# Optimization experiments

Hardware: AMD Instinct MI355X
Metric: run time of the kernel (lower is better)

## Reference

```python
import jax, jax.numpy as jnp
import numpy as np

N_NODES = 100000
N_EDGES = 1000000
IN_DIM = 128
OUT_DIM = 64
NEG_SLOPE = 0.2


def setup_inputs() -> dict:
    key = jax.random.key(0)
    k = jax.random.split(key, 6)
    h = jax.random.normal(k[0], (N_NODES, IN_DIM), dtype=jnp.float32)
    # xavier-uniform-ish scales for linear weights
    W_w = jax.random.uniform(k[1], (OUT_DIM, IN_DIM), dtype=jnp.float32,
                             minval=-1.0, maxval=1.0) * np.sqrt(6.0 / (IN_DIM + OUT_DIM))
    W_b = jnp.zeros((OUT_DIM,), dtype=jnp.float32)
    a_w = jax.random.uniform(k[2], (1, 2 * OUT_DIM), dtype=jnp.float32,
                             minval=-1.0, maxval=1.0) * np.sqrt(6.0 / (2 * OUT_DIM + 1))
    a_b = jnp.zeros((1,), dtype=jnp.float32)
    edge_index = jax.random.randint(k[3], (2, N_EDGES), 0, N_NODES, dtype=jnp.int64)
    return {"h": h, "W_w": W_w, "W_b": W_b, "a_w": a_w, "a_b": a_b,
            "edge_index": edge_index}


def reference(h, W_w, W_b, a_w, a_b, edge_index):
    # Wh = W(h): [N, D_out]
    Wh = h @ W_w.T + W_b
    src, tgt = edge_index[0], edge_index[1]
    D = Wh.shape[1]
    # a([e_src, e_tgt]) decomposes: score = Wh@a_src per-node + Wh@a_tgt per-node,
    # gathered by edge (avoids materializing the [E, 2D] concat).
    s_src = Wh @ a_w[0, :D]   # [N]
    s_tgt = Wh @ a_w[0, D:]   # [N]
    logits = jax.nn.leaky_relu(s_src[src] + s_tgt[tgt] + a_b[0], NEG_SLOPE)  # [E]
    # NOTE: global softmax over all edges (dim=0), faithful to the source.
    attn = jax.nn.softmax(logits, axis=0)
    e_src = Wh[src]  # [E, D] gather
    messages = jnp.zeros_like(Wh).at[tgt].add(attn[:, None] * e_src)  # scatter-add
    return jax.nn.leaky_relu(messages, NEG_SLOPE)
```

## Files before the change

kernel.cpp:

```cpp
#include <hip/hip_runtime.h>
#include <math.h>

#define N_NODES 100000
#define N_EDGES 1000000
#define IN_DIM  128
#define OUT_DIM 64
#define NEG     0.2f

#define SCAN_BLOCKS 391
#define EDGE_BLOCKS 3907

typedef __attribute__((ext_vector_type(8))) short short8;
typedef __attribute__((ext_vector_type(4))) float f32x4;

#define MFMA(A, B, C) __builtin_amdgcn_mfma_f32_16x16x32_bf16(A, B, C, 0, 0, 0)

union U16 { unsigned u[4]; short8 s; };

__device__ __forceinline__ void split8(const float* x, short8& hi, short8& lo) {
    U16 H, L;
#pragma unroll
    for (int i = 0; i < 4; ++i) {
        float a = x[2 * i], b = x[2 * i + 1];
        unsigned ua = __float_as_uint(a), ub = __float_as_uint(b);
        unsigned ha = ua & 0xffff0000u, hb = ub & 0xffff0000u;
        H.u[i] = (ua >> 16) | hb;
        float la = a - __uint_as_float(ha);
        float lb = b - __uint_as_float(hb);
        L.u[i] = (__float_as_uint(la) >> 16) | (__float_as_uint(lb) & 0xffff0000u);
    }
    hi = H.s; lo = L.s;
}

__global__ __launch_bounds__(256, 3) void k1_mfma(
    const float* __restrict__ h, const float* __restrict__ W,
    const float* __restrict__ Wb, const float* __restrict__ aw,
    float* __restrict__ Wh, float* __restrict__ s_src, float* __restrict__ s_tgt)
{
    __shared__ float4 smem4[2176];
    unsigned short* wfh = (unsigned short*)smem4;
    unsigned short* wfl = wfh + 8192;

    const int tid  = threadIdx.x;
    const int lane = tid & 63, w = tid >> 6;
    const int c = lane & 15, g = lane >> 4;
    const int n0 = blockIdx.x * 128;

#pragma unroll
    for (int it = 0; it < 4; ++it) {
        int U = tid + 256 * it;
        int pos = U >> 6, l = U & 63;
        int nb = pos >> 2, ks = pos & 3;
        int r  = 16 * nb + (l & 15);
        int k0 = 32 * ks + 8 * (l >> 4);
        float a[8];
        *(float4*)&a[0] = *(const float4*)(W + r * IN_DIM + k0);
        *(float4*)&a[4] = *(const float4*)(W + r * IN_DIM + k0 + 4);
        short8 hi, lo; split8(a, hi, lo);
        *(short8*)(wfh + (size_t)U * 8) = hi;
        *(short8*)(wfl + (size_t)U * 8) = lo;
    }
    __syncthreads();

    const int na0 = n0 + 32 * w + c;
    const float* hp0 = h + (size_t)min(na0, N_NODES - 1) * IN_DIM + 8 * g;
    const float* hp1 = h + (size_t)min(na0 + 16, N_NODES - 1) * IN_DIM + 8 * g;

    f32x4 acc[2][4];
    {
        f32x4 z = {0.f, 0.f, 0.f, 0.f};
#pragma unroll
        for (int m = 0; m < 2; ++m)
#pragma unroll
            for (int nb = 0; nb < 4; ++nb) acc[m][nb] = z;
    }

#pragma unroll 2
    for (int ks = 0; ks < 4; ++ks) {
        short8 bh[4], bl[4];
#pragma unroll
        for (int nb = 0; nb < 4; ++nb) {
            int u = ((nb * 4 + ks) * 64 + lane) * 8;
            bh[nb] = *(const short8*)(wfh + u);
            bl[nb] = *(const short8*)(wfl + u);
        }
        float am[8];
        short8 ah, al;
        *(float4*)&am[0] = *(const float4*)(hp0 + 32 * ks);
        *(float4*)&am[4] = *(const float4*)(hp0 + 32 * ks + 4);
        split8(am, ah, al);
#pragma unroll
        for (int nb = 0; nb < 4; ++nb) {
            acc[0][nb] = MFMA(ah, bh[nb], acc[0][nb]);
            acc[0][nb] = MFMA(ah, bl[nb], acc[0][nb]);
            acc[0][nb] = MFMA(al, bh[nb], acc[0][nb]);
        }
        *(float4*)&am[0] = *(const float4*)(hp1 + 32 * ks);
        *(float4*)&am[4] = *(const float4*)(hp1 + 32 * ks + 4);
        split8(am, ah, al);
#pragma unroll
        for (int nb = 0; nb < 4; ++nb) {
            acc[1][nb] = MFMA(ah, bh[nb], acc[1][nb]);
            acc[1][nb] = MFMA(ah, bl[nb], acc[1][nb]);
            acc[1][nb] = MFMA(al, bh[nb], acc[1][nb]);
        }
    }

    float wb[4], w1[4], w2[4];
#pragma unroll
    for (int nb = 0; nb < 4; ++nb) {
        wb[nb] = Wb[16 * nb + c];
        w1[nb] = aw[16 * nb + c];
        w2[nb] = aw[OUT_DIM + 16 * nb + c];
    }
#pragma unroll
    for (int m = 0; m < 2; ++m)
#pragma unroll
        for (int r = 0; r < 4; ++r) {
            float s1 = 0.f, s2 = 0.f;
#pragma unroll
            for (int nb = 0; nb < 4; ++nb) {
                float v = acc[m][nb][r] + wb[nb];
                acc[m][nb][r] = v;
                s1 = fmaf(v, w1[nb], s1);
                s2 = fmaf(v, w2[nb], s2);
            }
#pragma unroll
            for (int mk = 1; mk < 16; mk <<= 1) {
                s1 += __shfl_xor(s1, mk);
                s2 += __shfl_xor(s2, mk);
            }
            if (c == 0) {
                int node = n0 + 32 * w + 16 * m + 4 * g + r;
                if (node < N_NODES) { s_src[node] = s1; s_tgt[node] = s2; }
            }
        }

    __syncthreads();
    float* tr = (float*)smem4;
#pragma unroll
    for (int m = 0; m < 2; ++m)
#pragma unroll
        for (int nb = 0; nb < 4; ++nb)
#pragma unroll
            for (int r = 0; r < 4; ++r)
                tr[(32 * w + 16 * m + 4 * g + r) * 68 + 16 * nb + c] = acc[m][nb][r];
    __syncthreads();

#pragma unroll
    for (int j = 0; j < 8; ++j) {
        int idx = tid + 256 * j;
        int nloc = idx >> 4, d4 = idx & 15;
        int node = n0 + nloc;
        if (node < N_NODES)
            ((float4*)Wh)[(size_t)node * 16 + d4] =
                *(const float4*)&tr[nloc * 68 + d4 * 4];
    }
}

__global__ __launch_bounds__(256) void k2_fused(
    const int* __restrict__ ei, const float* __restrict__ s_src,
    const float* __restrict__ s_tgt, const float* __restrict__ ab,
    unsigned* __restrict__ deg, unsigned* __restrict__ rank,
    float* __restrict__ exv, float* __restrict__ bsum)
{
    const float ab0 = ab[0];
    float lsum = 0.f;
    const int e = blockIdx.x * blockDim.x + threadIdx.x;
    if (e < N_EDGES) {
        int s = ei[e], t = ei[N_EDGES + e];
        float x = s_src[s] + s_tgt[t] + ab0;
        float l = x > 0.f ? x : NEG * x;
        float ex = __expf(l);
        exv[e] = ex;
        lsum = ex;
        rank[e] = atomicAdd(&deg[t], 1u);
    }
#pragma unroll
    for (int off = 32; off; off >>= 1) lsum += __shfl_xor(lsum, off);
    __shared__ float ssum[4];
    if ((threadIdx.x & 63) == 0) ssum[threadIdx.x >> 6] = lsum;
    __syncthreads();
    if (threadIdx.x == 0)
        bsum[blockIdx.x] = ssum[0] + ssum[1] + ssum[2] + ssum[3];
}

__global__ __launch_bounds__(256) void k_scan1(
    const unsigned* __restrict__ deg, unsigned* __restrict__ psum)
{
    const int i = blockIdx.x * 256 + threadIdx.x;
    unsigned v = (i < N_NODES) ? deg[i] : 0u;
    unsigned w = v;
#pragma unroll
    for (int off = 32; off; off >>= 1) w += __shfl_xor(w, off);
    __shared__ unsigned ss[4];
    if ((threadIdx.x & 63) == 0) ss[threadIdx.x >> 6] = w;
    __syncthreads();
    if (threadIdx.x == 0) psum[blockIdx.x] = ss[0] + ss[1] + ss[2] + ss[3];
}

__global__ __launch_bounds__(512) void k_scan2(
    const unsigned* __restrict__ psum, unsigned* __restrict__ poff,
    const float* __restrict__ bsum, float* __restrict__ gsum)
{
    __shared__ unsigned sc[512];
    __shared__ float    sf[8];
    const int t = threadIdx.x;

    unsigned v = (t < SCAN_BLOCKS) ? psum[t] : 0u;
    sc[t] = v;
    __syncthreads();
    for (int off = 1; off < 512; off <<= 1) {
        unsigned u = (t >= off) ? sc[t - off] : 0u;
        __syncthreads();
        sc[t] += u;
        __syncthreads();
    }
    if (t < SCAN_BLOCKS) poff[t] = sc[t] - v;

    float s = 0.f;
    for (int i = t; i < EDGE_BLOCKS; i += 512) s += bsum[i];
#pragma unroll
    for (int off = 32; off; off >>= 1) s += __shfl_xor(s, off);
    if ((t & 63) == 0) sf[t >> 6] = s;
    __syncthreads();
    if (t == 0) {
        float tot = 0.f;
#pragma unroll
        for (int i = 0; i < 8; ++i) tot += sf[i];
        gsum[0] = tot;
    }
}

__global__ __launch_bounds__(256) void k_scan3(
    const unsigned* __restrict__ deg, const unsigned* __restrict__ poff,
    unsigned* __restrict__ row)
{
    __shared__ unsigned sc[256];
    const int t = threadIdx.x;
    const int i = blockIdx.x * 256 + t;
    unsigned v = (i < N_NODES) ? deg[i] : 0u;
    sc[t] = v;
    __syncthreads();
    for (int off = 1; off < 256; off <<= 1) {
        unsigned u = (t >= off) ? sc[t - off] : 0u;
        __syncthreads();
        sc[t] += u;
        __syncthreads();
    }
    unsigned r = poff[blockIdx.x] + sc[t] - v;
    if (i < N_NODES) row[i] = r;
    if (i == 0) row[N_NODES] = N_EDGES;
}

__global__ __launch_bounds__(256) void k3_fill(
    const int* __restrict__ ei, const float* __restrict__ exv,
    const unsigned* __restrict__ rank, const unsigned* __restrict__ row,
    int2* __restrict__ bin)
{
    const int e = blockIdx.x * blockDim.x + threadIdx.x;
    if (e >= N_EDGES) return;
    int t = ei[N_EDGES + e];
    unsigned pos = row[t] + rank[e];
    bin[pos] = make_int2(ei[e], __float_as_int(exv[e]));
}

__global__ __launch_bounds__(256) void k_gather(
    const unsigned* __restrict__ row, const int2* __restrict__ bin,
    const float* __restrict__ gsum, const float* __restrict__ Wh,
    float* __restrict__ out)
{
    const int lane = threadIdx.x & 63;
    const int t = blockIdx.x * 4 + (threadIdx.x >> 6);
    if (t >= N_NODES) return;
    const unsigned beg = row[t], end = row[t + 1];
    float a0 = 0.f, a1 = 0.f, a2 = 0.f, a3 = 0.f;
    for (unsigned base = beg; base < end; base += 64) {
        const int cnt = (int)min(64u, end - base);
        int2 p = make_int2(0, 0);
        if (lane < cnt) p = bin[base + lane];
        int j = 0;
        for (; j + 4 <= cnt; j += 4) {
            int   s0 = __shfl(p.x, j);     float w0 = __int_as_float(__shfl(p.y, j));
            int   s1 = __shfl(p.x, j + 1); float w1 = __int_as_float(__shfl(p.y, j + 1));
            int   s2 = __shfl(p.x, j + 2); float w2 = __int_as_float(__shfl(p.y, j + 2));
            int   s3 = __shfl(p.x, j + 3); float w3 = __int_as_float(__shfl(p.y, j + 3));
            float v0 = Wh[(size_t)s0 * OUT_DIM + lane];
            float v1 = Wh[(size_t)s1 * OUT_DIM + lane];
            float v2 = Wh[(size_t)s2 * OUT_DIM + lane];
            float v3 = Wh[(size_t)s3 * OUT_DIM + lane];
            a0 = fmaf(w0, v0, a0);
            a1 = fmaf(w1, v1, a1);
            a2 = fmaf(w2, v2, a2);
            a3 = fmaf(w3, v3, a3);
        }
        for (; j < cnt; ++j) {
            int   s = __shfl(p.x, j);
            float w = __int_as_float(__shfl(p.y, j));
            a0 = fmaf(w, Wh[(size_t)s * OUT_DIM + lane], a0);
        }
    }
    float v = ((a0 + a1) + (a2 + a3)) * (1.0f / gsum[0]);
    out[(size_t)t * OUT_DIM + lane] = v > 0.f ? v : NEG * v;
}

extern "C" void kernel_launch(void* const* d_in, const int* in_sizes, int n_in,
                              void* d_out, int out_size, void* d_ws, size_t ws_size,
                              hipStream_t stream)
{
    const float* h  = (const float*)d_in[0];
    const float* W  = (const float*)d_in[1];
    const float* Wb = (const float*)d_in[2];
    const float* aw = (const float*)d_in[3];
    const float* ab = (const float*)d_in[4];
    const int*   ei = (const int*)d_in[5];

    float* ws      = (float*)d_ws;
    float* Wh      = ws;
    float* s_src   = Wh + (size_t)N_NODES * OUT_DIM;
    float* s_tgt   = s_src + N_NODES;
    unsigned* deg    = (unsigned*)(s_tgt + N_NODES);
    unsigned* row    = deg + N_NODES;
    unsigned* psum   = row + N_NODES + 1;
    unsigned* poff   = psum + 512;
    int2*     bin    = (int2*)(poff + 512);
    float*    exv    = (float*)(bin + N_EDGES);
    unsigned* rank   = (unsigned*)(exv + N_EDGES);
    float*    bsum   = (float*)(rank + N_EDGES);
    float*    gsum   = bsum + 4096;

    float* out = (float*)d_out;

    hipMemsetAsync((void*)deg, 0, N_NODES * sizeof(unsigned), stream);

    k1_mfma<<<(N_NODES + 127) / 128, 256, 0, stream>>>(h, W, Wb, aw, Wh, s_src, s_tgt);
    k2_fused<<<EDGE_BLOCKS, 256, 0, stream>>>(ei, s_src, s_tgt, ab, deg, rank,
                                              exv, bsum);
    k_scan1<<<SCAN_BLOCKS, 256, 0, stream>>>(deg, psum);
    k_scan2<<<1, 512, 0, stream>>>(psum, poff, bsum, gsum);
    k_scan3<<<SCAN_BLOCKS, 256, 0, stream>>>(deg, poff, row);
    k3_fill<<<EDGE_BLOCKS, 256, 0, stream>>>(ei, exv, rank, row, bin);
    k_gather<<<(N_NODES + 3) / 4, 256, 0, stream>>>(row, bin, gsum, Wh, out);
}
```

Baseline: 224.2 us.

## Overlap degree-count atomics with GEMM and split counters into eight copies

The per-edge degree atomics move out of the score kernel and into the GEMM launch. One block in six runs the matmul and the rest count target degrees, so the atomic traffic overlaps with the MFMA work. The degree counter is replicated eight ways, keyed by edge-block mod 8, to cut atomic contention. Scan and fill are adapted with per-copy row offsets, and scan1 is folded into the score kernel. The cost is eight times the counter memset plus extra reads of the replicated counters and row offsets.

```diff
diff --git a/kernel.cpp b/kernel.cpp
--- a/kernel.cpp
+++ b/kernel.cpp
@@ -9,6 +9,8 @@
 
 #define SCAN_BLOCKS 391
 #define EDGE_BLOCKS 3907
+#define GEMM_BLOCKS 782
+#define FUSED_BLOCKS (GEMM_BLOCKS + EDGE_BLOCKS)
 
 typedef __attribute__((ext_vector_type(8))) short short8;
 typedef __attribute__((ext_vector_type(4))) float f32x4;
@@ -32,19 +34,32 @@
     hi = H.s; lo = L.s;
 }
 
-__global__ __launch_bounds__(256, 3) void k1_mfma(
+__global__ __launch_bounds__(256, 4) void kA_fused(
     const float* __restrict__ h, const float* __restrict__ W,
     const float* __restrict__ Wb, const float* __restrict__ aw,
-    float* __restrict__ Wh, float* __restrict__ s_src, float* __restrict__ s_tgt)
+    float* __restrict__ Wh, float* __restrict__ s_src, float* __restrict__ s_tgt,
+    const int* __restrict__ ei, unsigned* __restrict__ deg8,
+    unsigned* __restrict__ rank)
 {
     __shared__ float4 smem4[2176];
+
+    if ((blockIdx.x % 6) != 0) {
+        const int hid = blockIdx.x - blockIdx.x / 6 - 1;
+        const int e = hid * 256 + threadIdx.x;
+        if (e < N_EDGES) {
+            int t = ei[N_EDGES + e];
+            rank[e] = atomicAdd(&deg8[(size_t)(hid & 7) * N_NODES + t], 1u);
+        }
+        return;
+    }
+
     unsigned short* wfh = (unsigned short*)smem4;
     unsigned short* wfl = wfh + 8192;
 
     const int tid  = threadIdx.x;
     const int lane = tid & 63, w = tid >> 6;
     const int c = lane & 15, g = lane >> 4;
-    const int n0 = blockIdx.x * 128;
+    const int n0 = (blockIdx.x / 6) * 128;
 
 #pragma unroll
     for (int it = 0; it < 4; ++it) {
@@ -158,15 +173,16 @@
     }
 }
 
-__global__ __launch_bounds__(256) void k2_fused(
+__global__ __launch_bounds__(256) void k_mid(
     const int* __restrict__ ei, const float* __restrict__ s_src,
     const float* __restrict__ s_tgt, const float* __restrict__ ab,
-    unsigned* __restrict__ deg, unsigned* __restrict__ rank,
-    float* __restrict__ exv, float* __restrict__ bsum)
+    const unsigned* __restrict__ deg8,
+    float* __restrict__ exv, float* __restrict__ bsum,
+    unsigned* __restrict__ psum)
 {
     const float ab0 = ab[0];
     float lsum = 0.f;
-    const int e = blockIdx.x * blockDim.x + threadIdx.x;
+    const int e = blockIdx.x * 256 + threadIdx.x;
     if (e < N_EDGES) {
         int s = ei[e], t = ei[N_EDGES + e];
         float x = s_src[s] + s_tgt[t] + ab0;
@@ -174,7 +190,6 @@
         float ex = __expf(l);
         exv[e] = ex;
         lsum = ex;
-        rank[e] = atomicAdd(&deg[t], 1u);
     }
 #pragma unroll
     for (int off = 32; off; off >>= 1) lsum += __shfl_xor(lsum, off);
@@ -183,20 +198,22 @@
     __syncthreads();
     if (threadIdx.x == 0)
         bsum[blockIdx.x] = ssum[0] + ssum[1] + ssum[2] + ssum[3];
-}
-
-__global__ __launch_bounds__(256) void k_scan1(
-    const unsigned* __restrict__ deg, unsigned* __restrict__ psum)
-{
-    const int i = blockIdx.x * 256 + threadIdx.x;
-    unsigned v = (i < N_NODES) ? deg[i] : 0u;
-    unsigned w = v;
-#pragma unroll
-    for (int off = 32; off; off >>= 1) w += __shfl_xor(w, off);
-    __shared__ unsigned ss[4];
-    if ((threadIdx.x & 63) == 0) ss[threadIdx.x >> 6] = w;
-    __syncthreads();
-    if (threadIdx.x == 0) psum[blockIdx.x] = ss[0] + ss[1] + ss[2] + ss[3];
+
+    if (blockIdx.x < SCAN_BLOCKS) {
+        const int i = blockIdx.x * 256 + threadIdx.x;
+        unsigned v = 0;
+        if (i < N_NODES) {
+#pragma unroll
+            for (int x = 0; x < 8; ++x) v += deg8[(size_t)x * N_NODES + i];
+        }
+#pragma unroll
+        for (int off = 32; off; off >>= 1) v += __shfl_xor(v, off);
+        __shared__ unsigned us[4];
+        if ((threadIdx.x & 63) == 0) us[threadIdx.x >> 6] = v;
+        __syncthreads();
+        if (threadIdx.x == 0)
+            psum[blockIdx.x] = us[0] + us[1] + us[2] + us[3];
+    }
 }
 
 __global__ __launch_bounds__(512) void k_scan2(
@@ -233,14 +250,22 @@
 }
 
 __global__ __launch_bounds__(256) void k_scan3(
-    const unsigned* __restrict__ deg, const unsigned* __restrict__ poff,
-    unsigned* __restrict__ row)
+    const unsigned* __restrict__ deg8, const unsigned* __restrict__ poff,
+    unsigned* __restrict__ row, unsigned* __restrict__ row8)
 {
     __shared__ unsigned sc[256];
     const int t = threadIdx.x;
     const int i = blockIdx.x * 256 + t;
-    unsigned v = (i < N_NODES) ? deg[i] : 0u;
-    sc[t] = v;
+    unsigned d[8];
+    unsigned tot = 0;
+    if (i < N_NODES) {
+#pragma unroll
+        for (int x = 0; x < 8; ++x) {
+            d[x] = deg8[(size_t)x * N_NODES + i];
+            tot += d[x];
+        }
+    }
+    sc[t] = tot;
     __syncthreads();
     for (int off = 1; off < 256; off <<= 1) {
         unsigned u = (t >= off) ? sc[t - off] : 0u;
@@ -248,20 +273,29 @@
         sc[t] += u;
         __syncthreads();
     }
-    unsigned r = poff[blockIdx.x] + sc[t] - v;
-    if (i < N_NODES) row[i] = r;
+    if (i < N_NODES) {
+        unsigned base = poff[blockIdx.x] + sc[t] - tot;
+        row[i] = base;
+        unsigned run = base;
+#pragma unroll
+        for (int x = 0; x < 8; ++x) {
+            row8[(size_t)x * N_NODES + i] = run;
+            run += d[x];
+        }
+    }
     if (i == 0) row[N_NODES] = N_EDGES;
 }
 
 __global__ __launch_bounds__(256) void k3_fill(
     const int* __restrict__ ei, const float* __restrict__ exv,
-    const unsigned* __restrict__ rank, const unsigned* __restrict__ row,
+    const unsigned* __restrict__ rank, const unsigned* __restrict__ row8,
     int2* __restrict__ bin)
 {
     const int e = blockIdx.x * blockDim.x + threadIdx.x;
     if (e >= N_EDGES) return;
     int t = ei[N_EDGES + e];
-    unsigned pos = row[t] + rank[e];
+    int c = (e >> 8) & 7;
+    unsigned pos = row8[(size_t)c * N_NODES + t] + rank[e];
     bin[pos] = make_int2(ei[e], __float_as_int(exv[e]));
 }
 
@@ -319,9 +353,10 @@
     float* Wh      = ws;
     float* s_src   = Wh + (size_t)N_NODES * OUT_DIM;
     float* s_tgt   = s_src + N_NODES;
-    unsigned* deg    = (unsigned*)(s_tgt + N_NODES);
-    unsigned* row    = deg + N_NODES;
-    unsigned* psum   = row + N_NODES + 1;
+    unsigned* deg8   = (unsigned*)(s_tgt + N_NODES);
+    unsigned* row    = deg8 + (size_t)8 * N_NODES;
+    unsigned* row8   = row + N_NODES + 1;
+    unsigned* psum   = row8 + (size_t)8 * N_NODES;
     unsigned* poff   = psum + 512;
     int2*     bin    = (int2*)(poff + 512);
     float*    exv    = (float*)(bin + N_EDGES);
@@ -331,14 +366,14 @@
 
     float* out = (float*)d_out;
 
-    hipMemsetAsync((void*)deg, 0, N_NODES * sizeof(unsigned), stream);
-
-    k1_mfma<<<(N_NODES + 127) / 128, 256, 0, stream>>>(h, W, Wb, aw, Wh, s_src, s_tgt);
-    k2_fused<<<EDGE_BLOCKS, 256, 0, stream>>>(ei, s_src, s_tgt, ab, deg, rank,
-                                              exv, bsum);
-    k_scan1<<<SCAN_BLOCKS, 256, 0, stream>>>(deg, psum);
+    hipMemsetAsync((void*)deg8, 0, (size_t)8 * N_NODES * sizeof(unsigned), stream);
+
+    kA_fused<<<FUSED_BLOCKS, 256, 0, stream>>>(h, W, Wb, aw, Wh, s_src, s_tgt,
+                                               ei, deg8, rank);
+    k_mid<<<EDGE_BLOCKS, 256, 0, stream>>>(ei, s_src, s_tgt, ab, deg8,
+                                           exv, bsum, psum);
     k_scan2<<<1, 512, 0, stream>>>(psum, poff, bsum, gsum);
-    k_scan3<<<SCAN_BLOCKS, 256, 0, stream>>>(deg, poff, row);
-    k3_fill<<<EDGE_BLOCKS, 256, 0, stream>>>(ei, exv, rank, row, bin);
+    k_scan3<<<SCAN_BLOCKS, 256, 0, stream>>>(deg8, poff, row, row8);
+    k3_fill<<<EDGE_BLOCKS, 256, 0, stream>>>(ei, exv, rank, row8, bin);
     k_gather<<<(N_NODES + 3) / 4, 256, 0, stream>>>(row, bin, gsum, Wh, out);
 }
```

Result: slower. 228.7 us (+2.0%).
